# Optimization experiments

Measured on AMD Instinct MI355X. Metric: run time of the kernel, lower is better.

The kernel has to match this reference:

```python
import jax, jax.numpy as jnp
import numpy as np

B, S, HID, NH = 4, 1024, 1024, 16
HD = HID // NH  # 64


def setup_inputs() -> dict:
    key = jax.random.key(0)
    ks = jax.random.split(key, 8)
    scale = 0.02
    return {
        "attention_mask": jnp.zeros((B, 1, 1, S), dtype=jnp.float32),
        "query": jax.random.normal(ks[0], (B, S, HID), dtype=jnp.float32),
        "key": jax.random.normal(ks[1], (B, S, HID), dtype=jnp.float32),
        "value": jax.random.normal(ks[2], (B, S, HID), dtype=jnp.float32),
        "Wq": jax.random.normal(ks[3], (HID, HID), dtype=jnp.float32) * scale,
        "bq": jnp.zeros((HID,), dtype=jnp.float32),
        "Wk": jax.random.normal(ks[4], (HID, HID), dtype=jnp.float32) * scale,
        "bk": jnp.zeros((HID,), dtype=jnp.float32),
    }


def reference(attention_mask, query, key, value, Wq, bq, Wk, bk):
    # Linear projections (torch Linear: x @ W.T + b)
    q = query @ Wq.T + bq  # [B,S,HID]
    k = key @ Wk.T + bk    # [B,S,HID]
    # split heads -> [B,NH,S,HD]
    q = q.reshape(B, S, NH, HD).transpose(0, 2, 1, 3)
    k = k.reshape(B, S, NH, HD).transpose(0, 2, 1, 3)
    scores = jnp.einsum("bhqd,bhkd->bhqk", q, k) / jnp.sqrt(jnp.float32(HD))
    scores = scores + attention_mask  # additive mask broadcast [B,1,1,S]
    probs = jax.nn.softmax(scores, axis=-1)  # [B,NH,S,S]
    # V is shared across heads; head-mean folds into a single contraction:
    # mean_h(probs_h @ V) = (sum_h probs_h) @ V / NH
    out = jnp.einsum("bhqk,bkv->bqv", probs, value) / NH  # [B,S,HID]
    return out
```

## Files before the change

### kernel.cpp

```cpp
#include <hip/hip_runtime.h>
#include <hip/hip_fp16.h>

#define B_    4
#define S_    1024
#define HID_  1024
#define NH_   16
#define HD_   64

#define LOG2E 1.44269504f
#define PSTR  40

typedef _Float16 half8 __attribute__((ext_vector_type(8)));
typedef float f32x4 __attribute__((ext_vector_type(4)));

__device__ __forceinline__ half8 cvt8(float4 a, float4 b) {
    half8 h;
    h[0] = (_Float16)a.x; h[1] = (_Float16)a.y;
    h[2] = (_Float16)a.z; h[3] = (_Float16)a.w;
    h[4] = (_Float16)b.x; h[5] = (_Float16)b.y;
    h[6] = (_Float16)b.z; h[7] = (_Float16)b.w;
    return h;
}

__device__ __forceinline__ void gload_lds16(const void* g, void* l) {
    __builtin_amdgcn_global_load_lds(
        (const __attribute__((address_space(1))) unsigned int*)g,
        (__attribute__((address_space(3))) unsigned int*)l, 16, 0, 0);
}

__global__ __launch_bounds__(512) void proj_qk_f16(
    const float* __restrict__ query, const float* __restrict__ Wq,
    const float* __restrict__ bq, _Float16* __restrict__ Oq,
    const float* __restrict__ key, const float* __restrict__ Wk,
    const float* __restrict__ bk, _Float16* __restrict__ Ok)
{
    const float* A    = blockIdx.z ? key : query;
    const float* Wm   = blockIdx.z ? Wk  : Wq;
    const float* bias = blockIdx.z ? bk  : bq;
    _Float16* Co      = blockIdx.z ? Ok  : Oq;

    __shared__ _Float16 Al[128 * PSTR];
    __shared__ _Float16 Bl[128 * PSTR];

    const int tid  = threadIdx.x;
    const int wv   = tid >> 6;
    const int lane = tid & 63;
    const int l15  = lane & 15;
    const int quad = lane >> 4;
    const int wm   = wv & 1, wn = wv >> 1;
    const int m0   = blockIdx.y * 128, n0 = blockIdx.x * 128;
    const int sr   = tid >> 2;
    const int sc   = (tid & 3) * 8;

    f32x4 acc[4][2];
#pragma unroll
    for (int i = 0; i < 4; i++)
#pragma unroll
        for (int j = 0; j < 2; j++) acc[i][j] = (f32x4){0.f, 0.f, 0.f, 0.f};

    for (int kt = 0; kt < HID_; kt += 32) {
        const float* ap = A  + (long)(m0 + sr) * HID_ + kt + sc;
        const float* bp = Wm + (long)(n0 + sr) * HID_ + kt + sc;
        float4 av0 = *(const float4*)ap, av1 = *(const float4*)(ap + 4);
        float4 bv0 = *(const float4*)bp, bv1 = *(const float4*)(bp + 4);
        __syncthreads();
        *(half8*)(Al + sr * PSTR + sc) = cvt8(av0, av1);
        *(half8*)(Bl + sr * PSTR + sc) = cvt8(bv0, bv1);
        __syncthreads();

        half8 af[4], bfm[2];
#pragma unroll
        for (int i = 0; i < 4; i++)
            af[i] = *(const half8*)(Al + (wm * 64 + i * 16 + l15) * PSTR + quad * 8);
#pragma unroll
        for (int j = 0; j < 2; j++)
            bfm[j] = *(const half8*)(Bl + (wn * 32 + j * 16 + l15) * PSTR + quad * 8);
#pragma unroll
        for (int i = 0; i < 4; i++)
#pragma unroll
            for (int j = 0; j < 2; j++)
                acc[i][j] = __builtin_amdgcn_mfma_f32_16x16x32_f16(
                    af[i], bfm[j], acc[i][j], 0, 0, 0);
    }

    const int isQ = (blockIdx.z == 0);
#pragma unroll
    for (int j = 0; j < 2; j++) {
        int col = n0 + wn * 32 + j * 16 + l15;
        float bv = bias[col];
        int h = col >> 6, d = col & 63, p = d >> 3, jj = d & 7;
#pragma unroll
        for (int i = 0; i < 4; i++) {
            int row = m0 + wm * 64 + i * 16 + quad * 4;
            int bb = row >> 10, ss = row & 1023;
            long base;
            if (isQ)
                base = ((((long)(bb * NH_ + h) * 64 + (ss >> 4)) * 8 + p) * 16
                        + (ss & 15)) * 8 + jj;
            else
                base = (((long)(bb * NH_ + h) * 8 + p) * 1024 + ss) * 8 + jj;
#pragma unroll
            for (int r = 0; r < 4; r++)
                Co[base + r * 8] = (_Float16)(acc[i][j][r] + bv);
        }
    }
}

__global__ __launch_bounds__(512) void attn_psum_f16(
    const _Float16* __restrict__ qb,
    const _Float16* __restrict__ kb,
    const float* __restrict__ mask,
    _Float16* __restrict__ P)
{
    const int b    = blockIdx.y;
    const int qt   = blockIdx.x;
    const int q0   = qt * 16;
    const int hz   = blockIdx.z;
    const int tid  = threadIdx.x;
    const int w    = tid >> 6;
    const int lane = tid & 63;
    const int l15  = lane & 15;
    const int quad = lane >> 4;

    __shared__ float redS[2][16][8];

    const float SC = 0.125f * LOG2E;

    float mreg[8];
#pragma unroll
    for (int t = 0; t < 8; t++)
        mreg[t] = mask[b * S_ + t * 128 + w * 16 + l15] * LOG2E;

    f32x4 acc[8];
#pragma unroll
    for (int t = 0; t < 8; t++) acc[t] = (f32x4){0.f, 0.f, 0.f, 0.f};

    for (int ii = 0; ii < 4; ii++) {
        const int h = hz * 4 + ii;
        const _Float16* qh = qb + ((long)(b * NH_ + h) * 64 + qt) * 1024;
        const _Float16* kh = kb + (long)(b * NH_ + h) * 8192 * 8;

        half8 a0 = *(const half8*)(qh + quad * 128 + l15 * 8);
        half8 a1 = *(const half8*)(qh + (quad + 4) * 128 + l15 * 8);

        f32x4 s[8];
#pragma unroll
        for (int cc = 0; cc < 8; cc++) {
            const int key = cc * 128 + w * 16 + l15;
            half8 b0 = *(const half8*)(kh + (long)quad * 8192 + key * 8);
            half8 b1 = *(const half8*)(kh + (long)(quad + 4) * 8192 + key * 8);
            f32x4 c = (f32x4){0.f, 0.f, 0.f, 0.f};
            c = __builtin_amdgcn_mfma_f32_16x16x32_f16(a0, b0, c, 0, 0, 0);
            c = __builtin_amdgcn_mfma_f32_16x16x32_f16(a1, b1, c, 0, 0, 0);
            s[cc] = c;
        }

        const int p = ii & 1;
        float sm[4] = {0.f, 0.f, 0.f, 0.f};
#pragma unroll
        for (int t = 0; t < 8; t++)
#pragma unroll
            for (int r = 0; r < 4; r++) {
                float pr = exp2f(s[t][r] * SC + mreg[t]);
                s[t][r] = pr;
                sm[r] += pr;
            }
#pragma unroll
        for (int off = 1; off < 16; off <<= 1)
#pragma unroll
            for (int r = 0; r < 4; r++) sm[r] += __shfl_xor(sm[r], off);
        if (l15 == 0)
#pragma unroll
            for (int r = 0; r < 4; r++) redS[p][quad * 4 + r][w] = sm[r];
        __syncthreads();

#pragma unroll
        for (int r = 0; r < 4; r++) {
            float4 v0 = *(float4*)&redS[p][quad * 4 + r][0];
            float4 v1 = *(float4*)&redS[p][quad * 4 + r][4];
            float tot = (v0.x + v0.y + v0.z + v0.w) + (v1.x + v1.y + v1.z + v1.w);
            float inv = 1.f / tot;
#pragma unroll
            for (int t = 0; t < 8; t++) acc[t][r] += s[t][r] * inv;
        }
    }

    _Float16* prow = P + (long)hz * ((long)B_ * S_ * S_) + (long)(b * S_ + q0) * S_;
#pragma unroll
    for (int t = 0; t < 8; t++)
#pragma unroll
        for (int r = 0; r < 4; r++) {
            int row = quad * 4 + r;
            prow[(long)row * S_ + t * 128 + w * 16 + l15] = (_Float16)acc[t][r];
        }
}

__global__ __launch_bounds__(256) void vt_combine(
    const _Float16* __restrict__ P, _Float16* __restrict__ o,
    const float* __restrict__ V, _Float16* __restrict__ Vt)
{
    __shared__ float t[32][33];
    if (blockIdx.y == 0) {
        if (blockIdx.x >= 2048) return;
        const long QS = (long)B_ * S_ * S_;
        long i = (long)(blockIdx.x * 256 + threadIdx.x) * 8;
        half8 a = *(const half8*)(P + i);
        half8 b = *(const half8*)(P + QS + i);
        half8 c = *(const half8*)(P + 2 * QS + i);
        half8 d = *(const half8*)(P + 3 * QS + i);
        half8 r;
#pragma unroll
        for (int e = 0; e < 8; e++)
            r[e] = (_Float16)((float)a[e] + (float)b[e] + (float)c[e] + (float)d[e]);
        *(half8*)(o + i) = r;
    } else {
        const int x  = blockIdx.x;
        const int b  = x >> 10;
        const int s0 = ((x >> 5) & 31) * 32;
        const int h0 = (x & 31) * 32;
        const int tx = threadIdx.x & 31, ty = threadIdx.x >> 5;
#pragma unroll
        for (int rr = 0; rr < 4; rr++) {
            int s = s0 + ty + rr * 8;
            t[ty + rr * 8][tx] = V[((long)b * S_ + s) * HID_ + h0 + tx];
        }
        __syncthreads();
#pragma unroll
        for (int rr = 0; rr < 4; rr++) {
            int h = h0 + ty + rr * 8;
            Vt[((long)b * HID_ + h) * S_ + s0 + tx] = (_Float16)t[tx][ty + rr * 8];
        }
    }
}

__global__ __launch_bounds__(256) void pv_f16(
    const _Float16* __restrict__ Pc,
    const _Float16* __restrict__ Vt,
    float* __restrict__ out)
{
    const int b = blockIdx.z;
    const _Float16* A  = Pc + (long)b * S_ * S_;
    const _Float16* Bm = Vt + (long)b * HID_ * S_;

    __shared__ _Float16 Al[128 * PSTR];
    __shared__ _Float16 Bl[64 * PSTR];

    const int tid  = threadIdx.x;
    const int wv   = tid >> 6;
    const int lane = tid & 63;
    const int l15  = lane & 15;
    const int quad = lane >> 4;
    const int wm   = wv & 1, wn = wv >> 1;
    const int m0   = blockIdx.y * 128, n0 = blockIdx.x * 64;
    const int sr   = tid >> 2;
    const int sc   = (tid & 3) * 8;

    f32x4 acc[4][2];
#pragma unroll
    for (int i = 0; i < 4; i++)
#pragma unroll
        for (int j = 0; j < 2; j++) acc[i][j] = (f32x4){0.f, 0.f, 0.f, 0.f};

    for (int kt = 0; kt < S_; kt += 32) {
        half8 a0 = *(const half8*)(A  + (long)(m0 + sr) * S_ + kt + sc);
        half8 a1 = *(const half8*)(A  + (long)(m0 + 64 + sr) * S_ + kt + sc);
        half8 b0 = *(const half8*)(Bm + (long)(n0 + sr) * S_ + kt + sc);
        __syncthreads();
        *(half8*)(Al + sr * PSTR + sc) = a0;
        *(half8*)(Al + (64 + sr) * PSTR + sc) = a1;
        *(half8*)(Bl + sr * PSTR + sc) = b0;
        __syncthreads();

        half8 af[4], bfm[2];
#pragma unroll
        for (int i = 0; i < 4; i++)
            af[i] = *(const half8*)(Al + (wm * 64 + i * 16 + l15) * PSTR + quad * 8);
#pragma unroll
        for (int j = 0; j < 2; j++)
            bfm[j] = *(const half8*)(Bl + (wn * 32 + j * 16 + l15) * PSTR + quad * 8);
#pragma unroll
        for (int i = 0; i < 4; i++)
#pragma unroll
            for (int j = 0; j < 2; j++)
                acc[i][j] = __builtin_amdgcn_mfma_f32_16x16x32_f16(
                    af[i], bfm[j], acc[i][j], 0, 0, 0);
    }

    const float alpha = 1.f / NH_;
#pragma unroll
    for (int i = 0; i < 4; i++) {
        int row = m0 + wm * 64 + i * 16 + quad * 4;
#pragma unroll
        for (int j = 0; j < 2; j++) {
            int col = n0 + wn * 32 + j * 16 + l15;
#pragma unroll
            for (int r = 0; r < 4; r++)
                out[(long)(b * S_ + row + r) * HID_ + col] = acc[i][j][r] * alpha;
        }
    }
}

extern "C" void kernel_launch(void* const* d_in, const int* in_sizes, int n_in,
                              void* d_out, int out_size, void* d_ws, size_t ws_size,
                              hipStream_t stream)
{
    const float* mask  = (const float*)d_in[0];
    const float* query = (const float*)d_in[1];
    const float* key   = (const float*)d_in[2];
    const float* value = (const float*)d_in[3];
    const float* Wq    = (const float*)d_in[4];
    const float* bq    = (const float*)d_in[5];
    const float* Wk    = (const float*)d_in[6];
    const float* bk    = (const float*)d_in[7];
    float* out = (float*)d_out;

    char* ws = (char*)d_ws;
    const long MB = 1l << 20;
    _Float16* qbuf = (_Float16*)(ws);
    _Float16* kbuf = (_Float16*)(ws + 8 * MB);
    _Float16* Pq   = (_Float16*)(ws + 16 * MB);
    _Float16* Vt   = (_Float16*)(ws);
    _Float16* psum = (_Float16*)(ws + 8 * MB);

    proj_qk_f16<<<dim3(HID_ / 128, (B_ * S_) / 128, 2), dim3(512), 0, stream>>>(
        query, Wq, bq, qbuf, key, Wk, bk, kbuf);

    attn_psum_f16<<<dim3(S_ / 16, B_, 4), dim3(512), 0, stream>>>(
        qbuf, kbuf, mask, Pq);

    vt_combine<<<dim3(4096, 2), dim3(256), 0, stream>>>(Pq, psum, value, Vt);

    pv_f16<<<dim3(HID_ / 64, S_ / 128, B_), dim3(256), 0, stream>>>(psum, Vt, out);
}
```

Baseline: 211.6 us.

## Double-buffer LDS with register prefetch and swizzle block order in QK projection

```diff
diff --git a/kernel.cpp b/kernel.cpp
--- a/kernel.cpp
+++ b/kernel.cpp
@@ -22,25 +22,23 @@
     return h;
 }
 
-__device__ __forceinline__ void gload_lds16(const void* g, void* l) {
-    __builtin_amdgcn_global_load_lds(
-        (const __attribute__((address_space(1))) unsigned int*)g,
-        (__attribute__((address_space(3))) unsigned int*)l, 16, 0, 0);
-}
-
 __global__ __launch_bounds__(512) void proj_qk_f16(
     const float* __restrict__ query, const float* __restrict__ Wq,
     const float* __restrict__ bq, _Float16* __restrict__ Oq,
     const float* __restrict__ key, const float* __restrict__ Wk,
     const float* __restrict__ bk, _Float16* __restrict__ Ok)
 {
-    const float* A    = blockIdx.z ? key : query;
-    const float* Wm   = blockIdx.z ? Wk  : Wq;
-    const float* bias = blockIdx.z ? bk  : bq;
-    _Float16* Co      = blockIdx.z ? Ok  : Oq;
-
-    __shared__ _Float16 Al[128 * PSTR];
-    __shared__ _Float16 Bl[128 * PSTR];
+    const int f  = blockIdx.x + 8 * blockIdx.y + 256 * blockIdx.z;
+    const int w2 = (f & 7) * 64 + (f >> 3);
+    const int bx = w2 & 7, by = (w2 >> 3) & 31, bz = w2 >> 8;
+
+    const float* A    = bz ? key : query;
+    const float* Wm   = bz ? Wk  : Wq;
+    const float* bias = bz ? bk  : bq;
+    _Float16* Co      = bz ? Ok  : Oq;
+
+    __shared__ _Float16 Al[2][128 * PSTR];
+    __shared__ _Float16 Bl[2][128 * PSTR];
 
     const int tid  = threadIdx.x;
     const int wv   = tid >> 6;
@@ -48,42 +46,64 @@
     const int l15  = lane & 15;
     const int quad = lane >> 4;
     const int wm   = wv & 1, wn = wv >> 1;
-    const int m0   = blockIdx.y * 128, n0 = blockIdx.x * 128;
+    const int m0   = by * 128, n0 = bx * 128;
     const int sr   = tid >> 2;
     const int sc   = (tid & 3) * 8;
 
+    const float* ap = A  + (long)(m0 + sr) * HID_ + sc;
+    const float* bp = Wm + (long)(n0 + sr) * HID_ + sc;
+
     f32x4 acc[4][2];
 #pragma unroll
     for (int i = 0; i < 4; i++)
 #pragma unroll
         for (int j = 0; j < 2; j++) acc[i][j] = (f32x4){0.f, 0.f, 0.f, 0.f};
 
+    float4 a0 = *(const float4*)ap,       a1 = *(const float4*)(ap + 4);
+    float4 b0 = *(const float4*)bp,       b1 = *(const float4*)(bp + 4);
+    *(half8*)&Al[0][sr * PSTR + sc] = cvt8(a0, a1);
+    *(half8*)&Bl[0][sr * PSTR + sc] = cvt8(b0, b1);
+    a0 = *(const float4*)(ap + 32); a1 = *(const float4*)(ap + 36);
+    b0 = *(const float4*)(bp + 32); b1 = *(const float4*)(bp + 36);
+    __syncthreads();
+
+#pragma unroll 2
     for (int kt = 0; kt < HID_; kt += 32) {
-        const float* ap = A  + (long)(m0 + sr) * HID_ + kt + sc;
-        const float* bp = Wm + (long)(n0 + sr) * HID_ + kt + sc;
-        float4 av0 = *(const float4*)ap, av1 = *(const float4*)(ap + 4);
-        float4 bv0 = *(const float4*)bp, bv1 = *(const float4*)(bp + 4);
-        __syncthreads();
-        *(half8*)(Al + sr * PSTR + sc) = cvt8(av0, av1);
-        *(half8*)(Bl + sr * PSTR + sc) = cvt8(bv0, bv1);
-        __syncthreads();
+        const int p = (kt >> 5) & 1;
+
+        float4 na0 = a0, na1 = a1, nb0 = b0, nb1 = b1;
+        if (kt + 64 < HID_) {
+            na0 = *(const float4*)(ap + kt + 64);
+            na1 = *(const float4*)(ap + kt + 68);
+            nb0 = *(const float4*)(bp + kt + 64);
+            nb1 = *(const float4*)(bp + kt + 68);
+        }
 
         half8 af[4], bfm[2];
 #pragma unroll
         for (int i = 0; i < 4; i++)
-            af[i] = *(const half8*)(Al + (wm * 64 + i * 16 + l15) * PSTR + quad * 8);
+            af[i] = *(const half8*)(&Al[p][(wm * 64 + i * 16 + l15) * PSTR + quad * 8]);
 #pragma unroll
         for (int j = 0; j < 2; j++)
-            bfm[j] = *(const half8*)(Bl + (wn * 32 + j * 16 + l15) * PSTR + quad * 8);
+            bfm[j] = *(const half8*)(&Bl[p][(wn * 32 + j * 16 + l15) * PSTR + quad * 8]);
+
+        if (kt + 32 < HID_) {
+            *(half8*)&Al[p ^ 1][sr * PSTR + sc] = cvt8(a0, a1);
+            *(half8*)&Bl[p ^ 1][sr * PSTR + sc] = cvt8(b0, b1);
+        }
+
 #pragma unroll
         for (int i = 0; i < 4; i++)
 #pragma unroll
             for (int j = 0; j < 2; j++)
                 acc[i][j] = __builtin_amdgcn_mfma_f32_16x16x32_f16(
                     af[i], bfm[j], acc[i][j], 0, 0, 0);
-    }
-
-    const int isQ = (blockIdx.z == 0);
+
+        __syncthreads();
+        a0 = na0; a1 = na1; b0 = nb0; b1 = nb1;
+    }
+
+    const int isQ = (bz == 0);
 #pragma unroll
     for (int j = 0; j < 2; j++) {
         int col = n0 + wn * 32 + j * 16 + l15;
```

Result: no change. 209.8 us (-0.9%).
